# Kernel tuning notes

Hardware: AMD Instinct MI355X
Metric: run time of the kernel (lower is better)

The kernel has to match this reference:

```python
import jax, jax.numpy as jnp
import numpy as np

EPS = 1e-4


def setup_inputs() -> dict:
    key = jax.random.key(0)
    ks = jax.random.split(key, 9)
    B, N, OBS, PRED, IN, E, C, K = 2048, 64, 8, 12, 6, 512, 6, 20
    d_self = IN * (OBS + PRED)  # 120
    d_nei = IN * OBS            # 48
    obs = jax.random.normal(ks[0], (B, OBS, IN), dtype=jnp.float32)
    neis = jax.random.normal(ks[1], (B, N, OBS, IN), dtype=jnp.float32)
    self_labels = jax.random.randint(ks[2], (B,), 0, C)
    nei_labels = jax.random.randint(ks[3], (B, N), 0, C + 1)
    init_trajs = jax.random.normal(ks[4], (C, K, PRED, IN), dtype=jnp.float32)
    # per-class Linear params, stored [in, out] (torch Linear is x @ W.T + b)
    W_self = jax.random.normal(ks[5], (C, d_self, E), dtype=jnp.float32) * (1.0 / np.sqrt(d_self))
    b_self = jax.random.normal(ks[6], (C, E), dtype=jnp.float32) * 0.02
    W_nei = jax.random.normal(ks[7], (C + 1, d_nei, E), dtype=jnp.float32) * (1.0 / np.sqrt(d_nei))
    b_nei = jax.random.normal(ks[8], (C + 1, E), dtype=jnp.float32) * 0.02
    return {"obs": obs, "neis": neis, "init_trajs": init_trajs,
            "W_self": W_self, "b_self": b_self, "W_nei": W_nei, "b_nei": b_nei,
            "self_labels": self_labels, "nei_labels": nei_labels}


def reference(obs, neis, init_trajs, W_self, b_self, W_nei, b_nei, self_labels, nei_labels):
    B = obs.shape[0]
    N = neis.shape[1]
    C, _, E = W_self.shape
    Cn = W_nei.shape[0]  # num_class + 1

    # gather per-sample anchor trajectories: [B, K, pred_len, in_size]
    it = init_trajs[self_labels]
    K = it.shape[1]
    obs_r = jnp.broadcast_to(obs[:, None], (B, K) + obs.shape[1:])
    traj = jnp.concatenate([obs_r, it], axis=2).reshape(B, K, -1)  # [B, K, in*(obs+pred)]

    # label-conditioned self embedding: loop over small fixed class count
    x = jnp.zeros((B, K, E), dtype=traj.dtype)
    for c in range(C):
        out_c = traj @ W_self[c] + b_self[c]
        x = jnp.where((self_labels == c)[:, None, None], out_c, x)

    # elementwise signed-reciprocal transform on neighbor features
    neis_f = neis.reshape(B, N, -1)  # [B, N, in*obs]
    neis_t = jnp.where(neis_f >= 0, 1.0 / (neis_f + EPS), 1.0 / (neis_f - EPS))

    # label-conditioned neighbor embedding over num_class+1 classes
    nei_feats = jnp.zeros((B, N, E), dtype=neis_t.dtype)
    for c in range(Cn):
        out_c = neis_t @ W_nei[c] + b_nei[c]
        nei_feats = jnp.where((nei_labels == c)[:, :, None], out_c, nei_feats)

    return x, nei_feats
```

## Files before the change

kernel.cpp:

```cpp
#include <hip/hip_runtime.h>
#include <hip/hip_bf16.h>

#define B_    2048
#define N_    64
#define E_    512
#define K_    20
#define C_    6
#define DSELF 120
#define DNEI  48
#define DPRED 72
#define EPS_  1e-4f

__global__ __launch_bounds__(256) void self_embed(
    const float* __restrict__ obs,
    const float* __restrict__ init_trajs,
    const float* __restrict__ W_self,
    const float* __restrict__ b_self,
    const int*   __restrict__ labels,
    float*       __restrict__ out)
{
    const int b   = blockIdx.x;
    const int tid = threadIdx.x;
    const int c   = labels[b];

    __shared__ __align__(16) float traj[DSELF * K_];

    for (int idx = tid; idx < DSELF * K_; idx += 256) {
        const int j = idx / K_;
        const int k = idx - j * K_;
        float v;
        if (j < DNEI) v = obs[b * DNEI + j];
        else          v = init_trajs[(c * K_ + k) * DPRED + (j - DNEI)];
        traj[idx] = v;
    }
    __syncthreads();

    float acc[K_][2];
    #pragma unroll
    for (int k = 0; k < K_; ++k) { acc[k][0] = 0.f; acc[k][1] = 0.f; }

    const float2* Wp = reinterpret_cast<const float2*>(W_self + (size_t)c * DSELF * E_) + tid;

    for (int j = 0; j < DSELF; ++j) {
        const float2 w  = Wp[j * (E_ / 2)];
        const float4* tp = reinterpret_cast<const float4*>(&traj[j * K_]);
        #pragma unroll
        for (int q = 0; q < 5; ++q) {
            const float4 t4 = tp[q];
            acc[q * 4 + 0][0] += t4.x * w.x; acc[q * 4 + 0][1] += t4.x * w.y;
            acc[q * 4 + 1][0] += t4.y * w.x; acc[q * 4 + 1][1] += t4.y * w.y;
            acc[q * 4 + 2][0] += t4.z * w.x; acc[q * 4 + 2][1] += t4.z * w.y;
            acc[q * 4 + 3][0] += t4.w * w.x; acc[q * 4 + 3][1] += t4.w * w.y;
        }
    }

    const float2 bs = reinterpret_cast<const float2*>(b_self + c * E_)[tid];
    #pragma unroll
    for (int k = 0; k < K_; ++k) {
        float2 o;
        o.x = acc[k][0] + bs.x;
        o.y = acc[k][1] + bs.y;
        reinterpret_cast<float2*>(out + (size_t)(b * K_ + k) * E_)[tid] = o;
    }
}

__global__ __launch_bounds__(256) void nei_embed(
    const float* __restrict__ neis,
    const float* __restrict__ W_nei,
    const float* __restrict__ b_nei,
    const int*   __restrict__ labels,
    float*       __restrict__ out)
{
    const int b   = blockIdx.x;
    const int tid = threadIdx.x;

    __shared__ __align__(16) float nt[N_ * DNEI];
    __shared__ int lab[N_];

    if (tid < N_) lab[tid] = labels[b * N_ + tid];

    const float4* np4 = reinterpret_cast<const float4*>(neis + (size_t)b * N_ * DNEI);
    float4* nt4 = reinterpret_cast<float4*>(nt);
    #pragma unroll
    for (int i = 0; i < 3; ++i) {
        const int idx = tid + i * 256;
        float4 v = np4[idx];
        float4 o;
        o.x = (v.x >= 0.f) ? 1.f / (v.x + EPS_) : 1.f / (v.x - EPS_);
        o.y = (v.y >= 0.f) ? 1.f / (v.y + EPS_) : 1.f / (v.y - EPS_);
        o.z = (v.z >= 0.f) ? 1.f / (v.z + EPS_) : 1.f / (v.z - EPS_);
        o.w = (v.w >= 0.f) ? 1.f / (v.w + EPS_) : 1.f / (v.w - EPS_);
        nt4[idx] = o;
    }
    __syncthreads();

    float wl[DNEI], wh[DNEI];

    for (int c = 0; c < C_ + 1; ++c) {
        const float2* Wp = reinterpret_cast<const float2*>(W_nei + (size_t)c * DNEI * E_) + tid;
        #pragma unroll
        for (int j = 0; j < DNEI; ++j) {
            const float2 w = Wp[j * (E_ / 2)];
            wl[j] = w.x;
            wh[j] = w.y;
        }
        const float2 bs = reinterpret_cast<const float2*>(b_nei + c * E_)[tid];

        for (int n = 0; n < N_; ++n) {
            if (lab[n] != c) continue;
            float a0 = bs.x, a1 = bs.y;
            const float4* tp = reinterpret_cast<const float4*>(&nt[n * DNEI]);
            #pragma unroll
            for (int q = 0; q < 12; ++q) {
                const float4 t4 = tp[q];
                a0 += t4.x * wl[q * 4 + 0]; a1 += t4.x * wh[q * 4 + 0];
                a0 += t4.y * wl[q * 4 + 1]; a1 += t4.y * wh[q * 4 + 1];
                a0 += t4.z * wl[q * 4 + 2]; a1 += t4.z * wh[q * 4 + 2];
                a0 += t4.w * wl[q * 4 + 3]; a1 += t4.w * wh[q * 4 + 3];
            }
            float2 o; o.x = a0; o.y = a1;
            reinterpret_cast<float2*>(out + (size_t)(b * N_ + n) * E_)[tid] = o;
        }
    }
}

extern "C" void kernel_launch(void* const* d_in, const int* in_sizes, int n_in,
                              void* d_out, int out_size, void* d_ws, size_t ws_size,
                              hipStream_t stream) {
    const float* obs  = (const float*)d_in[0];
    const float* neis = (const float*)d_in[1];
    const float* it   = (const float*)d_in[2];
    const float* Ws   = (const float*)d_in[3];
    const float* bs   = (const float*)d_in[4];
    const float* Wn   = (const float*)d_in[5];
    const float* bn   = (const float*)d_in[6];
    const int* sl = (const int*)d_in[7];
    const int* nl = (const int*)d_in[8];

    float* out_x = (float*)d_out;
    float* out_n = out_x + (size_t)B_ * K_ * E_;

    self_embed<<<dim3(B_), dim3(256), 0, stream>>>(obs, it, Ws, bs, sl, out_x);
    nei_embed<<<dim3(B_), dim3(256), 0, stream>>>(neis, Wn, bn, nl, out_n);
}
```

Baseline: 555.4 us.

## Split self embedding into per-class anchor term plus per-sample obs term

The self embedding is decomposed algebraically. The init_trajs part of the matmul depends only on (class, k), so it is precomputed once into a C*K*E table in workspace. Each sample then only does a 48-long dot product and adds the table rows. The neighbor reciprocal transform moves into the same prep kernel, which writes its results to workspace, so the neighbor GEMM reads pre-transformed rows from global memory. This cuts the self-embedding FLOPs sharply, at the cost of an extra launch, workspace traffic, and uncached global row reads in nei_gemm. The new path needs enough workspace and falls back to the old kernels otherwise.

```diff
diff --git a/kernel.cpp b/kernel.cpp
--- a/kernel.cpp
+++ b/kernel.cpp
@@ -1,5 +1,4 @@
 #include <hip/hip_runtime.h>
-#include <hip/hip_bf16.h>
 
 #define B_    2048
 #define N_    64
@@ -11,7 +10,132 @@
 #define DPRED 72
 #define EPS_  1e-4f
 
-__global__ __launch_bounds__(256) void self_embed(
+#define C2_ELEMS ((size_t)C_ * K_ * E_)
+#define NT_ELEMS ((size_t)B_ * N_ * DNEI)
+#define WS_NEED  ((C2_ELEMS + NT_ELEMS) * sizeof(float))
+
+#define TBLOCKS 1536
+
+__global__ __launch_bounds__(256) void prep(
+    const float* __restrict__ neis,
+    const float* __restrict__ init_trajs,
+    const float* __restrict__ W_self,
+    const float* __restrict__ b_self,
+    float*       __restrict__ ws)
+{
+    const int tid = threadIdx.x;
+    const int bid = blockIdx.x;
+    if (bid < C_ * K_) {
+        const int c = bid / K_;
+        const float* itr = init_trajs + (size_t)bid * DPRED;
+        const float2* Wp = reinterpret_cast<const float2*>(
+                               W_self + ((size_t)c * DSELF + DNEI) * E_) + tid;
+        float2 acc = reinterpret_cast<const float2*>(b_self + (size_t)c * E_)[tid];
+        #pragma unroll
+        for (int j = 0; j < DPRED; ++j) {
+            const float t  = itr[j];
+            const float2 w = Wp[(size_t)j * (E_ / 2)];
+            acc.x += t * w.x; acc.y += t * w.y;
+        }
+        reinterpret_cast<float2*>(ws + (size_t)bid * E_)[tid] = acc;
+    } else {
+        const int ib = bid - C_ * K_;
+        const size_t base   = (size_t)ib * 256 + tid;
+        const size_t stride = (size_t)TBLOCKS * 256;
+        const float4* in4 = reinterpret_cast<const float4*>(neis);
+        float4* o4 = reinterpret_cast<float4*>(ws + C2_ELEMS);
+        #pragma unroll
+        for (int t = 0; t < 4; ++t) {
+            const size_t idx = base + (size_t)t * stride;
+            const float4 v = in4[idx];
+            float4 o;
+            o.x = (v.x >= 0.f) ? 1.f / (v.x + EPS_) : 1.f / (v.x - EPS_);
+            o.y = (v.y >= 0.f) ? 1.f / (v.y + EPS_) : 1.f / (v.y - EPS_);
+            o.z = (v.z >= 0.f) ? 1.f / (v.z + EPS_) : 1.f / (v.z - EPS_);
+            o.w = (v.w >= 0.f) ? 1.f / (v.w + EPS_) : 1.f / (v.w - EPS_);
+            o4[idx] = o;
+        }
+    }
+}
+
+__global__ __launch_bounds__(256) void self_fast(
+    const float* __restrict__ obs,
+    const float* __restrict__ W_self,
+    const int*   __restrict__ labels,
+    const float* __restrict__ c2,
+    float*       __restrict__ out)
+{
+    const int b   = blockIdx.x;
+    const int tid = threadIdx.x;
+    const int c   = labels[b];
+
+    const float*  ob = obs + (size_t)b * DNEI;
+    const float2* Wp = reinterpret_cast<const float2*>(
+                           W_self + (size_t)c * DSELF * E_) + tid;
+    float ax = 0.f, ay = 0.f;
+    #pragma unroll
+    for (int j = 0; j < DNEI; ++j) {
+        const float t  = ob[j];
+        const float2 w = Wp[(size_t)j * (E_ / 2)];
+        ax += t * w.x; ay += t * w.y;
+    }
+
+    const float2* cp = reinterpret_cast<const float2*>(
+                           c2 + (size_t)c * K_ * E_) + tid;
+    float2* op = reinterpret_cast<float2*>(out + (size_t)b * K_ * E_) + tid;
+    #pragma unroll
+    for (int k = 0; k < K_; ++k) {
+        const float2 v = cp[(size_t)k * (E_ / 2)];
+        float2 o; o.x = ax + v.x; o.y = ay + v.y;
+        op[(size_t)k * (E_ / 2)] = o;
+    }
+}
+
+__global__ __launch_bounds__(256) void nei_gemm(
+    const float* __restrict__ nts,
+    const float* __restrict__ W_nei,
+    const float* __restrict__ b_nei,
+    const int*   __restrict__ labels,
+    float*       __restrict__ out)
+{
+    const int b   = blockIdx.x;
+    const int tid = threadIdx.x;
+
+    __shared__ int lab[N_];
+    if (tid < N_) lab[tid] = labels[b * N_ + tid];
+    __syncthreads();
+
+    float wl[DNEI], wh[DNEI];
+
+    for (int c = 0; c < C_ + 1; ++c) {
+        const float2* Wp = reinterpret_cast<const float2*>(
+                               W_nei + (size_t)c * DNEI * E_) + tid;
+        #pragma unroll
+        for (int j = 0; j < DNEI; ++j) {
+            const float2 w = Wp[(size_t)j * (E_ / 2)];
+            wl[j] = w.x;
+            wh[j] = w.y;
+        }
+        const float2 bs = reinterpret_cast<const float2*>(
+                              b_nei + (size_t)c * E_)[tid];
+
+        for (int n = 0; n < N_; ++n) {
+            if (lab[n] != c) continue;
+            const float* r = nts + ((size_t)b * N_ + n) * DNEI;
+            float a0 = bs.x, a1 = bs.y;
+            #pragma unroll
+            for (int j = 0; j < DNEI; ++j) {
+                const float t = r[j];
+                a0 += t * wl[j];
+                a1 += t * wh[j];
+            }
+            float2 o; o.x = a0; o.y = a1;
+            reinterpret_cast<float2*>(out + ((size_t)b * N_ + n) * E_)[tid] = o;
+        }
+    }
+}
+
+__global__ __launch_bounds__(256) void self_embed_fb(
     const float* __restrict__ obs,
     const float* __restrict__ init_trajs,
     const float* __restrict__ W_self,
@@ -64,7 +188,7 @@
     }
 }
 
-__global__ __launch_bounds__(256) void nei_embed(
+__global__ __launch_bounds__(256) void nei_embed_fb(
     const float* __restrict__ neis,
     const float* __restrict__ W_nei,
     const float* __restrict__ b_nei,
@@ -140,6 +264,14 @@
     float* out_x = (float*)d_out;
     float* out_n = out_x + (size_t)B_ * K_ * E_;
 
-    self_embed<<<dim3(B_), dim3(256), 0, stream>>>(obs, it, Ws, bs, sl, out_x);
-    nei_embed<<<dim3(B_), dim3(256), 0, stream>>>(neis, Wn, bn, nl, out_n);
-}
+    if (d_ws != nullptr && ws_size >= WS_NEED) {
+        float* c2 = (float*)d_ws;
+        float* nt = c2 + C2_ELEMS;
+        prep<<<dim3(C_ * K_ + TBLOCKS), dim3(256), 0, stream>>>(neis, it, Ws, bs, (float*)d_ws);
+        self_fast<<<dim3(B_), dim3(256), 0, stream>>>(obs, Ws, sl, c2, out_x);
+        nei_gemm<<<dim3(B_), dim3(256), 0, stream>>>(nt, Wn, bn, nl, out_n);
+    } else {
+        self_embed_fb<<<dim3(B_), dim3(256), 0, stream>>>(obs, it, Ws, bs, sl, out_x);
+        nei_embed_fb<<<dim3(B_), dim3(256), 0, stream>>>(neis, Wn, bn, nl, out_n);
+    }
+}
```

Result: slower. 617.8 us (+11.2%).
